# Performance work log

Measured on AMD Instinct MI355X. Metric: run time of the kernel, lower is better.

Reference implementation:

```python
import jax, jax.numpy as jnp
import numpy as np

D = 256       # d_model
NH = 8        # heads
K = 7         # neighborhood kernel size
DFF = 1024    # feedforward dim
EPS = 1e-5
B, H, W = 4, 56, 56


def layer_norm(x, g, b):
    m = jnp.mean(x, axis=-1, keepdims=True)
    v = jnp.mean((x - m) ** 2, axis=-1, keepdims=True)
    return (x - m) * jax.lax.rsqrt(v + EPS) * g + b


def neighborhood_attn(x, W_qkv, b_qkv, W_proj, b_proj):
    # NATTEN NeighborhoodAttention2D: each query attends to a KxK window
    # centered on it, clamped (shifted) at borders so every query sees K*K keys.
    Bx, Hx, Wx, C = x.shape
    hd = C // NH
    qkv = x @ W_qkv + b_qkv                      # [B,H,W,3C]
    q, k, v = jnp.split(qkv, 3, axis=-1)
    q = q.reshape(Bx, Hx, Wx, NH, hd)
    k = k.reshape(Bx, Hx, Wx, NH, hd)
    v = v.reshape(Bx, Hx, Wx, NH, hd)
    # neighbor index grids: start = clip(i - K//2, 0, H-K), window = start + [0..K)
    ih = jnp.clip(jnp.arange(Hx) - K // 2, 0, Hx - K)[:, None] + jnp.arange(K)  # [H,K]
    iw = jnp.clip(jnp.arange(Wx) - K // 2, 0, Wx - K)[:, None] + jnp.arange(K)  # [W,K]
    # gather K/V neighborhoods -> [B,H,W,K,K,NH,hd]
    k_nb = k[:, ih[:, None, :, None], iw[None, :, None, :]]
    v_nb = v[:, ih[:, None, :, None], iw[None, :, None, :]]
    attn = jnp.einsum('bhwnd,bhwijnd->bhwnij', q, k_nb) * (hd ** -0.5)
    attn = jax.nn.softmax(attn.reshape(Bx, Hx, Wx, NH, K * K), axis=-1)
    attn = attn.reshape(Bx, Hx, Wx, NH, K, K)
    out = jnp.einsum('bhwnij,bhwijnd->bhwnd', attn, v_nb).reshape(Bx, Hx, Wx, C)
    return out @ W_proj + b_proj


def setup_inputs() -> dict:
    key = jax.random.key(0)
    ks = jax.random.split(key, 8)
    s = 0.02
    return {
        'x': jax.random.normal(ks[0], (B, H, W, D), dtype=jnp.float32),
        'W_qkv': jax.random.normal(ks[1], (D, 3 * D), dtype=jnp.float32) * s,
        'b_qkv': jnp.zeros((3 * D,), dtype=jnp.float32),
        'W_proj': jax.random.normal(ks[2], (D, D), dtype=jnp.float32) * s,
        'b_proj': jnp.zeros((D,), dtype=jnp.float32),
        'W1': jax.random.normal(ks[3], (D, DFF), dtype=jnp.float32) * s,
        'b1': jnp.zeros((DFF,), dtype=jnp.float32),
        'W2': jax.random.normal(ks[4], (DFF, D), dtype=jnp.float32) * s,
        'b2': jnp.zeros((D,), dtype=jnp.float32),
        'g1': jnp.ones((D,), dtype=jnp.float32),
        'be1': jnp.zeros((D,), dtype=jnp.float32),
        'g2': jnp.ones((D,), dtype=jnp.float32),
        'be2': jnp.zeros((D,), dtype=jnp.float32),
    }


def reference(x, W_qkv, b_qkv, W_proj, b_proj, W1, b1, W2, b2, g1, be1, g2, be2):
    # norm_first=False (post-norm): x = norm1(x + mha(x)); x = norm2(x + ff(x))
    a = neighborhood_attn(x, W_qkv, b_qkv, W_proj, b_proj)
    x = layer_norm(x + a, g1, be1)
    f = jax.nn.relu(x @ W1 + b1) @ W2 + b2
    return layer_norm(x + f, g2, be2)
```

## Files before the change

### kernel.cpp

```cpp
#include <hip/hip_runtime.h>
#include <math.h>

#define BATCH 4
#define HH 56
#define WW 56
#define DMODEL 256
#define NHEADS 8
#define HD 32
#define NNB 49
#define NTOK (BATCH*HH*WW)

#define HALO 22
#define NHTOK (HALO*HALO)
#define KV_PAD 40

typedef __attribute__((ext_vector_type(8))) short s16x8;
typedef __attribute__((ext_vector_type(4))) float f32x4;
typedef __attribute__((ext_vector_type(2))) float f32x2;

__device__ inline unsigned short f2b(float f) {
    union { float f; unsigned int u; } v; v.f = f;
    unsigned int r = v.u + 0x7FFF + ((v.u >> 16) & 1);
    return (unsigned short)(r >> 16);
}
__device__ inline float b2f(unsigned short u) {
    union { float f; unsigned int u; } v; v.u = ((unsigned int)u) << 16;
    return v.f;
}

__device__ __forceinline__ f32x2 unpk(unsigned int u) {
    union { unsigned int u; float f; } lo, hi;
    lo.u = u << 16;
    hi.u = u & 0xffff0000u;
    return f32x2{lo.f, hi.f};
}

__device__ __forceinline__ f32x2 pk_fma(f32x2 a, f32x2 b, f32x2 c) {
#if __has_builtin(__builtin_elementwise_fma)
    return __builtin_elementwise_fma(a, b, c);
#else
    return f32x2{fmaf(a.x, b.x, c.x), fmaf(a.y, b.y, c.y)};
#endif
}

__device__ __forceinline__ void async16(const unsigned short* g, unsigned short* l) {
    __builtin_amdgcn_global_load_lds(
        (const __attribute__((address_space(1))) unsigned int*)g,
        (__attribute__((address_space(3))) unsigned int*)l, 16, 0, 0);
}

#define XCAST_BLOCKS 1568

__device__ __forceinline__ void transpose_tile(
    const float* __restrict__ src, unsigned short* __restrict__ dst,
    int K, int N, int kt, int nt, int tid, float* lds )
{
    const int k0 = kt * 64, n0 = nt * 64;
    #pragma unroll
    for (int p = 0; p < 4; ++p) {
        const int r  = p * 16 + (tid >> 4);
        const int c4 = (tid & 15) * 4;
        const float4 v = *(const float4*)(src + (size_t)(k0 + r) * N + n0 + c4);
        lds[r * 65 + c4 + 0] = v.x; lds[r * 65 + c4 + 1] = v.y;
        lds[r * 65 + c4 + 2] = v.z; lds[r * 65 + c4 + 3] = v.w;
    }
    __syncthreads();
    #pragma unroll
    for (int p = 0; p < 4; ++p) {
        const int c  = p * 16 + (tid >> 4);
        const int k4 = (tid & 15) * 4;
        ushort4 o;
        o.x = f2b(lds[(k4 + 0) * 65 + c]);
        o.y = f2b(lds[(k4 + 1) * 65 + c]);
        o.z = f2b(lds[(k4 + 2) * 65 + c]);
        o.w = f2b(lds[(k4 + 3) * 65 + c]);
        *(ushort4*)(dst + (size_t)(n0 + c) * K + k0 + k4) = o;
    }
}

__global__ __launch_bounds__(256)
void prep_kernel(const float* __restrict__ x,
                 const float* __restrict__ Wq, const float* __restrict__ Wp,
                 const float* __restrict__ W1, const float* __restrict__ W2,
                 unsigned short* __restrict__ xb,
                 unsigned short* __restrict__ Wqb, unsigned short* __restrict__ Wpb,
                 unsigned short* __restrict__ W1b, unsigned short* __restrict__ W2b)
{
    __shared__ float lds[64 * 65];
    const int tid = threadIdx.x;
    if (blockIdx.x < XCAST_BLOCKS) {
        const int i = blockIdx.x * 256 + tid;
        const float4* xp = (const float4*)x + (size_t)i * 2;
        const float4 a = xp[0], b = xp[1];
        s16x8 o;
        o[0] = (short)f2b(a.x); o[1] = (short)f2b(a.y);
        o[2] = (short)f2b(a.z); o[3] = (short)f2b(a.w);
        o[4] = (short)f2b(b.x); o[5] = (short)f2b(b.y);
        o[6] = (short)f2b(b.z); o[7] = (short)f2b(b.w);
        *((s16x8*)xb + i) = o;
        return;
    }
    int wb = blockIdx.x - XCAST_BLOCKS;
    if (wb < 48) {
        transpose_tile(Wq, Wqb, 256, 768, wb & 3, wb >> 2, tid, lds);
    } else if ((wb -= 48) < 16) {
        transpose_tile(Wp, Wpb, 256, 256, wb & 3, wb >> 2, tid, lds);
    } else if ((wb -= 16) < 64) {
        transpose_tile(W1, W1b, 256, 1024, wb & 3, wb >> 2, tid, lds);
    } else {
        wb -= 64;
        transpose_tile(W2, W2b, 1024, 256, wb & 15, wb >> 4, tid, lds);
    }
}

template<int BN>
__global__ __launch_bounds__(256)
void gemm_k(const unsigned short* __restrict__ Ab,
            const unsigned short* __restrict__ Bt, const float* __restrict__ bias,
            float* __restrict__ outf, unsigned short* __restrict__ outb,
            int M, int N, int K, int relu)
{
    constexpr int NB  = BN / 32;
    constexpr int BPW = BN / 32;
    __shared__ unsigned short As[2][128 * 64];
    __shared__ unsigned short Bs[2][BN * 64];

    const int tid = threadIdx.x;
    const int bm = blockIdx.y * 128, bn = blockIdx.x * BN;
    const int wid = tid >> 6, lane = tid & 63;
    const int wm = (wid >> 1) * 64, wn = (wid & 1) * (BN / 2);
    const int row16 = lane & 15, quad = lane >> 4;
    const int crow = lane >> 3, ck8 = (lane & 7) * 8;

    f32x4 acc[4][NB] = {};

    auto stage = [&](int buf, int k0) {
        #pragma unroll
        for (int c = 0; c < 4; ++c) {
            const int ch = wid * 4 + c;
            async16(Ab + (size_t)(bm + ch * 8 + crow) * K + k0 + ck8, As[buf] + ch * 512);
        }
        #pragma unroll
        for (int c = 0; c < BPW; ++c) {
            const int ch = wid * BPW + c;
            async16(Bt + (size_t)(bn + ch * 8 + crow) * K + k0 + ck8, Bs[buf] + ch * 512);
        }
    };
    auto compute = [&](int buf) {
        #pragma unroll
        for (int kc = 0; kc < 2; ++kc) {
            s16x8 af[4], bf[NB];
            #pragma unroll
            for (int i = 0; i < 4; ++i)
                af[i] = *(const s16x8*)(As[buf] + (wm + i * 16 + row16) * 64 + kc * 32 + quad * 8);
            #pragma unroll
            for (int j = 0; j < NB; ++j)
                bf[j] = *(const s16x8*)(Bs[buf] + (wn + j * 16 + row16) * 64 + kc * 32 + quad * 8);
            #pragma unroll
            for (int i = 0; i < 4; ++i)
                #pragma unroll
                for (int j = 0; j < NB; ++j)
                    acc[i][j] = __builtin_amdgcn_mfma_f32_16x16x32_bf16(af[i], bf[j], acc[i][j], 0, 0, 0);
        }
    };

    stage(0, 0);
    __syncthreads();
    for (int k0 = 0; k0 < K; k0 += 128) {
        stage(1, k0 + 64);
        compute(0);
        __syncthreads();
        if (k0 + 128 < K) stage(0, k0 + 128);
        compute(1);
        __syncthreads();
    }

    #pragma unroll
    for (int j = 0; j < NB; ++j) {
        const int col = bn + wn + j * 16 + row16;
        const float bb = bias[col];
        #pragma unroll
        for (int i = 0; i < 4; ++i) {
            const int r0 = bm + wm + i * 16 + quad * 4;
            #pragma unroll
            for (int reg = 0; reg < 4; ++reg) {
                float v = acc[i][j][reg] + bb;
                if (relu) v = fmaxf(v, 0.f);
                if (outf) outf[(size_t)(r0 + reg) * N + col] = v;
                if (outb) outb[(size_t)(r0 + reg) * N + col] = f2b(v);
            }
        }
    }
}

__global__ __launch_bounds__(512)
void gemm_ln(const unsigned short* __restrict__ Ab, const unsigned short* __restrict__ Bt,
             const float* __restrict__ bias, const float* __restrict__ resid,
             const float* __restrict__ g, const float* __restrict__ beta,
             float* __restrict__ outf, unsigned short* __restrict__ outb, int K)
{
    __shared__ unsigned short As[2][64 * 64];
    __shared__ unsigned short Bs[2][256 * 64];

    const int tid = threadIdx.x;
    const int bm = blockIdx.x * 64;
    const int wid = tid >> 6, lane = tid & 63;
    const int wm = (wid >> 2) * 32, wn = (wid & 3) * 64;
    const int wc = wid & 3;
    const int row16 = lane & 15, quad = lane >> 4;
    const int crow = lane >> 3, ck8 = (lane & 7) * 8;

    f32x4 acc[2][4] = {};

    auto stage = [&](int buf, int k0) {
        #pragma unroll
        for (int c = 0; c < 5; ++c) {
            const int ch = wid * 5 + c;
            if (ch < 8) {
                async16(Ab + (size_t)(bm + ch * 8 + crow) * K + k0 + ck8, As[buf] + ch * 512);
            } else {
                const int bc = ch - 8;
                async16(Bt + (size_t)(bc * 8 + crow) * K + k0 + ck8, Bs[buf] + bc * 512);
            }
        }
    };
    auto compute = [&](int buf) {
        #pragma unroll
        for (int kc = 0; kc < 2; ++kc) {
            s16x8 af[2], bf[4];
            #pragma unroll
            for (int i = 0; i < 2; ++i)
                af[i] = *(const s16x8*)(As[buf] + (wm + i * 16 + row16) * 64 + kc * 32 + quad * 8);
            #pragma unroll
            for (int j = 0; j < 4; ++j)
                bf[j] = *(const s16x8*)(Bs[buf] + (wn + j * 16 + row16) * 64 + kc * 32 + quad * 8);
            #pragma unroll
            for (int i = 0; i < 2; ++i)
                #pragma unroll
                for (int j = 0; j < 4; ++j)
                    acc[i][j] = __builtin_amdgcn_mfma_f32_16x16x32_bf16(af[i], bf[j], acc[i][j], 0, 0, 0);
        }
    };

    stage(0, 0);
    __syncthreads();
    for (int k0 = 0; k0 < K; k0 += 128) {
        stage(1, k0 + 64);
        compute(0);
        __syncthreads();
        if (k0 + 128 < K) stage(0, k0 + 128);
        compute(1);
        __syncthreads();
    }

    float bb[4], gv[4], bev[4];
    #pragma unroll
    for (int j = 0; j < 4; ++j) {
        const int col = wn + j * 16 + row16;
        bb[j] = bias[col]; gv[j] = g[col]; bev[j] = beta[col];
    }
    #pragma unroll
    for (int i = 0; i < 2; ++i) {
        #pragma unroll
        for (int reg = 0; reg < 4; ++reg) {
            const size_t rb = (size_t)(bm + wm + i * 16 + quad * 4 + reg) * 256;
            #pragma unroll
            for (int j = 0; j < 4; ++j)
                acc[i][j][reg] += bb[j] + resid[rb + wn + j * 16 + row16];
        }
    }

    float* red = (float*)As[0];
    #pragma unroll
    for (int i = 0; i < 2; ++i) {
        #pragma unroll
        for (int reg = 0; reg < 4; ++reg) {
            float s1 = 0.f, s2 = 0.f;
            #pragma unroll
            for (int j = 0; j < 4; ++j) {
                const float t = acc[i][j][reg];
                s1 += t; s2 += t * t;
            }
            #pragma unroll
            for (int o = 1; o < 16; o <<= 1) {
                s1 += __shfl_xor(s1, o, 64);
                s2 += __shfl_xor(s2, o, 64);
            }
            if (row16 == 0) {
                const int lrow = wm + i * 16 + quad * 4 + reg;
                red[lrow * 8 + wc * 2]     = s1;
                red[lrow * 8 + wc * 2 + 1] = s2;
            }
        }
    }
    __syncthreads();
    float* stats = red + 512;
    if (tid < 64) {
        const float S1 = red[tid*8] + red[tid*8+2] + red[tid*8+4] + red[tid*8+6];
        const float S2 = red[tid*8+1] + red[tid*8+3] + red[tid*8+5] + red[tid*8+7];
        const float m = S1 * (1.0f / 256.0f);
        const float var = S2 * (1.0f / 256.0f) - m * m;
        stats[tid * 2]     = m;
        stats[tid * 2 + 1] = rsqrtf(var + 1e-5f);
    }
    __syncthreads();

    #pragma unroll
    for (int i = 0; i < 2; ++i) {
        #pragma unroll
        for (int reg = 0; reg < 4; ++reg) {
            const int lrow = wm + i * 16 + quad * 4 + reg;
            const float m = stats[lrow * 2], r = stats[lrow * 2 + 1];
            const size_t rb = (size_t)(bm + lrow) * 256;
            #pragma unroll
            for (int j = 0; j < 4; ++j) {
                const int col = wn + j * 16 + row16;
                const float o = (acc[i][j][reg] - m) * r * gv[j] + bev[j];
                outf[rb + col] = o;
                if (outb) outb[rb + col] = f2b(o);
            }
        }
    }
}

__global__ __launch_bounds__(256, 2)
void natt_kernel(const unsigned short* __restrict__ qkvb, unsigned short* __restrict__ att)
{
    const int blk  = blockIdx.x;
    const int head = blk & 7;
    const int t2   = blk >> 3;
    const int tile = t2 & 15;
    const int b    = t2 >> 4;
    const int r0 = (tile >> 2) * 16, c0 = (tile & 3) * 16;
    const int hs = min(max(r0 - 3, 0), 34);
    const int ws = min(max(c0 - 3, 0), 34);

    __shared__ unsigned short Ks[NHTOK * KV_PAD];
    __shared__ unsigned short Vs[NHTOK * KV_PAD];

    const int tid = threadIdx.x;

    #pragma unroll
    for (int it = 0; it < 8; ++it) {
        const int t = it * 64 + (tid >> 2);
        if (t < NHTOK) {
            const int hr = t / HALO, hc = t - hr * HALO;
            const size_t rb = ((size_t)((b * 56 + hs + hr) * 56 + (ws + hc))) * 768;
            const int d8 = (tid & 3) * 8;
            *(s16x8*)(Ks + t * KV_PAD + d8) = *(const s16x8*)(qkvb + rb + 256 + head * 32 + d8);
            *(s16x8*)(Vs + t * KV_PAD + d8) = *(const s16x8*)(qkvb + rb + 512 + head * 32 + d8);
        }
    }

    const int qh = min(r0 + (tid >> 4), 55);
    const int qw = min(c0 + (tid & 15), 55);
    const int tok = (b * 56 + qh) * 56 + qw;
    const int ro = min(max(qh - 3, 0), 49) - hs;
    const int co = min(max(qw - 3, 0), 49) - ws;

    f32x2 qf[16];
    {
        const unsigned int* qp = (const unsigned int*)(qkvb + (size_t)tok * 768 + head * 32);
        #pragma unroll
        for (int p = 0; p < 16; ++p)
            qf[p] = unpk(qp[p]) * 0.17677669529663687f;
    }
    __syncthreads();

    f32x2 acc[16] = {};
    float sum = 0.f;
    for (int i = 0; i < 7; ++i) {
        const int trow = (ro + i) * HALO + co;
        #pragma unroll
        for (int j = 0; j < 7; ++j) {
            const unsigned int* kp = (const unsigned int*)(Ks + (trow + j) * KV_PAD);
            const unsigned int* vp = (const unsigned int*)(Vs + (trow + j) * KV_PAD);
            const uint4 ka = *(const uint4*)(kp);
            const uint4 kb = *(const uint4*)(kp + 4);
            const uint4 kc = *(const uint4*)(kp + 8);
            const uint4 kd = *(const uint4*)(kp + 12);
            const uint4 va = *(const uint4*)(vp);
            const uint4 vb = *(const uint4*)(vp + 4);
            const uint4 vc = *(const uint4*)(vp + 8);
            const uint4 vd = *(const uint4*)(vp + 12);
            f32x2 sa = {0.f, 0.f}, sb = {0.f, 0.f};
            sa = pk_fma(qf[0],  unpk(ka.x), sa);  sb = pk_fma(qf[1],  unpk(ka.y), sb);
            sa = pk_fma(qf[2],  unpk(ka.z), sa);  sb = pk_fma(qf[3],  unpk(ka.w), sb);
            sa = pk_fma(qf[4],  unpk(kb.x), sa);  sb = pk_fma(qf[5],  unpk(kb.y), sb);
            sa = pk_fma(qf[6],  unpk(kb.z), sa);  sb = pk_fma(qf[7],  unpk(kb.w), sb);
            sa = pk_fma(qf[8],  unpk(kc.x), sa);  sb = pk_fma(qf[9],  unpk(kc.y), sb);
            sa = pk_fma(qf[10], unpk(kc.z), sa);  sb = pk_fma(qf[11], unpk(kc.w), sb);
            sa = pk_fma(qf[12], unpk(kd.x), sa);  sb = pk_fma(qf[13], unpk(kd.y), sb);
            sa = pk_fma(qf[14], unpk(kd.z), sa);  sb = pk_fma(qf[15], unpk(kd.w), sb);
            const float p = __expf(sa.x + sa.y + sb.x + sb.y);
            sum += p;
            const f32x2 pv = {p, p};
            acc[0]  = pk_fma(pv, unpk(va.x), acc[0]);
            acc[1]  = pk_fma(pv, unpk(va.y), acc[1]);
            acc[2]  = pk_fma(pv, unpk(va.z), acc[2]);
            acc[3]  = pk_fma(pv, unpk(va.w), acc[3]);
            acc[4]  = pk_fma(pv, unpk(vb.x), acc[4]);
            acc[5]  = pk_fma(pv, unpk(vb.y), acc[5]);
            acc[6]  = pk_fma(pv, unpk(vb.z), acc[6]);
            acc[7]  = pk_fma(pv, unpk(vb.w), acc[7]);
            acc[8]  = pk_fma(pv, unpk(vc.x), acc[8]);
            acc[9]  = pk_fma(pv, unpk(vc.y), acc[9]);
            acc[10] = pk_fma(pv, unpk(vc.z), acc[10]);
            acc[11] = pk_fma(pv, unpk(vc.w), acc[11]);
            acc[12] = pk_fma(pv, unpk(vd.x), acc[12]);
            acc[13] = pk_fma(pv, unpk(vd.y), acc[13]);
            acc[14] = pk_fma(pv, unpk(vd.z), acc[14]);
            acc[15] = pk_fma(pv, unpk(vd.w), acc[15]);
        }
    }
    const float inv = 1.0f / sum;

    unsigned short* op = att + (size_t)tok * DMODEL + head * 32;
    #pragma unroll
    for (int d4 = 0; d4 < 8; ++d4) {
        ushort4 o;
        o.x = f2b(acc[d4 * 2].x     * inv);
        o.y = f2b(acc[d4 * 2].y     * inv);
        o.z = f2b(acc[d4 * 2 + 1].x * inv);
        o.w = f2b(acc[d4 * 2 + 1].y * inv);
        *(ushort4*)(op + d4 * 4) = o;
    }
}

extern "C" void kernel_launch(void* const* d_in, const int* in_sizes, int n_in,
                              void* d_out, int out_size, void* d_ws, size_t ws_size,
                              hipStream_t stream)
{
    const float* x      = (const float*)d_in[0];
    const float* W_qkv  = (const float*)d_in[1];
    const float* b_qkv  = (const float*)d_in[2];
    const float* W_proj = (const float*)d_in[3];
    const float* b_proj = (const float*)d_in[4];
    const float* W1     = (const float*)d_in[5];
    const float* b1     = (const float*)d_in[6];
    const float* W2     = (const float*)d_in[7];
    const float* b2     = (const float*)d_in[8];
    const float* g1     = (const float*)d_in[9];
    const float* be1    = (const float*)d_in[10];
    const float* g2     = (const float*)d_in[11];
    const float* be2    = (const float*)d_in[12];
    float* out = (float*)d_out;

    char* ws = (char*)d_ws;
    const int M = NTOK;

    unsigned short* qkvb = (unsigned short*)ws;
    unsigned short* h    = (unsigned short*)ws;
    unsigned short* attb = (unsigned short*)(ws + 38535168);
    float*          xn   = (float*)(ws + 57802752);
    unsigned short* xnb  = (unsigned short*)(ws + 70647808);
    unsigned short* Wqb  = (unsigned short*)(ws + 77070336);
    unsigned short* Wpb  = Wqb + 196608;
    unsigned short* W1b  = Wpb + 65536;
    unsigned short* W2b  = W1b + 262144;
    unsigned short* xb   = (unsigned short*)(ws + 78643200);

    dim3 blk(256);

    prep_kernel<<<dim3(XCAST_BLOCKS + 48 + 16 + 64 + 64), blk, 0, stream>>>(
        x, W_qkv, W_proj, W1, W2, xb, Wqb, Wpb, W1b, W2b);

    gemm_k<128><<<dim3(6, 98), blk, 0, stream>>>(xb, Wqb, b_qkv, nullptr, qkvb, M, 768, 256, 0);

    natt_kernel<<<dim3(512), blk, 0, stream>>>(qkvb, attb);

    gemm_ln<<<dim3(M / 64), dim3(512), 0, stream>>>(attb, Wpb, b_proj, x, g1, be1, xn, xnb, 256);

    gemm_k<128><<<dim3(8, 98), blk, 0, stream>>>(xnb, W1b, b1, nullptr, h, M, 1024, 256, 1);

    gemm_ln<<<dim3(M / 64), dim3(512), 0, stream>>>(h, W2b, b2, xn, g2, be2, out, nullptr, 1024);
}
```

Measured before the change: 194.8 us.

## Swizzle GEMM LDS tiles, remap blocks per XCD, stage epilogue through LDS

XOR-swizzles the 16-byte chunks of the LDS A/B tiles in both GEMM kernels so the fragment reads avoid bank conflicts. Remaps the 1D grid so consecutive tiles land on the same XCD, aiming for better L2 reuse of shared A/B rows. The bf16 epilogue of gemm_k now writes to LDS first, then stores coalesced 16-byte vectors to global memory, replacing scattered 2-byte stores. This costs an extra barrier and LDS pass, and the template parameter and fp32 output path are dropped.

```diff
diff --git a/kernel.cpp b/kernel.cpp
--- a/kernel.cpp
+++ b/kernel.cpp
@@ -113,53 +113,60 @@
     }
 }
 
-template<int BN>
 __global__ __launch_bounds__(256)
 void gemm_k(const unsigned short* __restrict__ Ab,
             const unsigned short* __restrict__ Bt, const float* __restrict__ bias,
-            float* __restrict__ outf, unsigned short* __restrict__ outb,
-            int M, int N, int K, int relu)
-{
-    constexpr int NB  = BN / 32;
-    constexpr int BPW = BN / 32;
+            unsigned short* __restrict__ outb,
+            int N, int K, int relu)
+{
     __shared__ unsigned short As[2][128 * 64];
-    __shared__ unsigned short Bs[2][BN * 64];
+    __shared__ unsigned short Bs[2][128 * 64];
 
     const int tid = threadIdx.x;
-    const int bm = blockIdx.y * 128, bn = blockIdx.x * BN;
+
+    const int nwg = gridDim.x;
+    const int q8 = nwg >> 3, r8 = nwg & 7;
+    const int xcd = blockIdx.x & 7, pos = blockIdx.x >> 3;
+    const int d = (xcd < r8 ? xcd * (q8 + 1) : r8 * (q8 + 1) + (xcd - r8) * q8) + pos;
+    const int nbx = N >> 7;
+    const int bm = (d / nbx) * 128, bn = (d % nbx) * 128;
+
     const int wid = tid >> 6, lane = tid & 63;
-    const int wm = (wid >> 1) * 64, wn = (wid & 1) * (BN / 2);
+    const int wm = (wid >> 1) * 64, wn = (wid & 1) * 64;
     const int row16 = lane & 15, quad = lane >> 4;
-    const int crow = lane >> 3, ck8 = (lane & 7) * 8;
-
-    f32x4 acc[4][NB] = {};
+    const int crow = lane >> 3;
+    const int ckS = ((lane & 7) ^ crow) * 8;
+
+    f32x4 acc[4][4] = {};
 
     auto stage = [&](int buf, int k0) {
         #pragma unroll
         for (int c = 0; c < 4; ++c) {
             const int ch = wid * 4 + c;
-            async16(Ab + (size_t)(bm + ch * 8 + crow) * K + k0 + ck8, As[buf] + ch * 512);
-        }
-        #pragma unroll
-        for (int c = 0; c < BPW; ++c) {
-            const int ch = wid * BPW + c;
-            async16(Bt + (size_t)(bn + ch * 8 + crow) * K + k0 + ck8, Bs[buf] + ch * 512);
+            async16(Ab + (size_t)(bm + ch * 8 + crow) * K + k0 + ckS, As[buf] + ch * 512);
+        }
+        #pragma unroll
+        for (int c = 0; c < 4; ++c) {
+            const int ch = wid * 4 + c;
+            async16(Bt + (size_t)(bn + ch * 8 + crow) * K + k0 + ckS, Bs[buf] + ch * 512);
         }
     };
     auto compute = [&](int buf) {
         #pragma unroll
         for (int kc = 0; kc < 2; ++kc) {
-            s16x8 af[4], bf[NB];
+            s16x8 af[4], bf[4];
             #pragma unroll
             for (int i = 0; i < 4; ++i)
-                af[i] = *(const s16x8*)(As[buf] + (wm + i * 16 + row16) * 64 + kc * 32 + quad * 8);
-            #pragma unroll
-            for (int j = 0; j < NB; ++j)
-                bf[j] = *(const s16x8*)(Bs[buf] + (wn + j * 16 + row16) * 64 + kc * 32 + quad * 8);
+                af[i] = *(const s16x8*)(As[buf] + (wm + i * 16 + row16) * 64
+                                        + (((kc * 4 + quad) ^ (row16 & 7)) * 8));
+            #pragma unroll
+            for (int j = 0; j < 4; ++j)
+                bf[j] = *(const s16x8*)(Bs[buf] + (wn + j * 16 + row16) * 64
+                                        + (((kc * 4 + quad) ^ (row16 & 7)) * 8));
             #pragma unroll
             for (int i = 0; i < 4; ++i)
                 #pragma unroll
-                for (int j = 0; j < NB; ++j)
+                for (int j = 0; j < 4; ++j)
                     acc[i][j] = __builtin_amdgcn_mfma_f32_16x16x32_bf16(af[i], bf[j], acc[i][j], 0, 0, 0);
         }
     };
@@ -175,21 +182,28 @@
         __syncthreads();
     }
 
-    #pragma unroll
-    for (int j = 0; j < NB; ++j) {
-        const int col = bn + wn + j * 16 + row16;
-        const float bb = bias[col];
+    unsigned short* Cs = (unsigned short*)As;
+    #pragma unroll
+    for (int j = 0; j < 4; ++j) {
+        const int col = wn + j * 16 + row16;
+        const float bb = bias[bn + col];
         #pragma unroll
         for (int i = 0; i < 4; ++i) {
-            const int r0 = bm + wm + i * 16 + quad * 4;
+            const int rr = wm + i * 16 + quad * 4;
             #pragma unroll
             for (int reg = 0; reg < 4; ++reg) {
                 float v = acc[i][j][reg] + bb;
                 if (relu) v = fmaxf(v, 0.f);
-                if (outf) outf[(size_t)(r0 + reg) * N + col] = v;
-                if (outb) outb[(size_t)(r0 + reg) * N + col] = f2b(v);
-            }
-        }
+                Cs[(rr + reg) * 128 + col] = f2b(v);
+            }
+        }
+    }
+    __syncthreads();
+    #pragma unroll
+    for (int p = 0; p < 8; ++p) {
+        const int s = p * 256 + tid;
+        const int rr = s >> 4, cb = (s & 15) * 8;
+        *(s16x8*)(outb + (size_t)(bm + rr) * N + bn + cb) = *(const s16x8*)(Cs + rr * 128 + cb);
     }
 }
 
@@ -208,7 +222,8 @@
     const int wm = (wid >> 2) * 32, wn = (wid & 3) * 64;
     const int wc = wid & 3;
     const int row16 = lane & 15, quad = lane >> 4;
-    const int crow = lane >> 3, ck8 = (lane & 7) * 8;
+    const int crow = lane >> 3;
+    const int ckS = ((lane & 7) ^ crow) * 8;
 
     f32x4 acc[2][4] = {};
 
@@ -217,10 +232,10 @@
         for (int c = 0; c < 5; ++c) {
             const int ch = wid * 5 + c;
             if (ch < 8) {
-                async16(Ab + (size_t)(bm + ch * 8 + crow) * K + k0 + ck8, As[buf] + ch * 512);
+                async16(Ab + (size_t)(bm + ch * 8 + crow) * K + k0 + ckS, As[buf] + ch * 512);
             } else {
                 const int bc = ch - 8;
-                async16(Bt + (size_t)(bc * 8 + crow) * K + k0 + ck8, Bs[buf] + bc * 512);
+                async16(Bt + (size_t)(bc * 8 + crow) * K + k0 + ckS, Bs[buf] + bc * 512);
             }
         }
     };
@@ -230,10 +245,12 @@
             s16x8 af[2], bf[4];
             #pragma unroll
             for (int i = 0; i < 2; ++i)
-                af[i] = *(const s16x8*)(As[buf] + (wm + i * 16 + row16) * 64 + kc * 32 + quad * 8);
+                af[i] = *(const s16x8*)(As[buf] + (wm + i * 16 + row16) * 64
+                                        + (((kc * 4 + quad) ^ (row16 & 7)) * 8));
             #pragma unroll
             for (int j = 0; j < 4; ++j)
-                bf[j] = *(const s16x8*)(Bs[buf] + (wn + j * 16 + row16) * 64 + kc * 32 + quad * 8);
+                bf[j] = *(const s16x8*)(Bs[buf] + (wn + j * 16 + row16) * 64
+                                        + (((kc * 4 + quad) ^ (row16 & 7)) * 8));
             #pragma unroll
             for (int i = 0; i < 2; ++i)
                 #pragma unroll
@@ -465,13 +482,13 @@
     prep_kernel<<<dim3(XCAST_BLOCKS + 48 + 16 + 64 + 64), blk, 0, stream>>>(
         x, W_qkv, W_proj, W1, W2, xb, Wqb, Wpb, W1b, W2b);
 
-    gemm_k<128><<<dim3(6, 98), blk, 0, stream>>>(xb, Wqb, b_qkv, nullptr, qkvb, M, 768, 256, 0);
+    gemm_k<<<dim3(6 * 98), blk, 0, stream>>>(xb, Wqb, b_qkv, qkvb, 768, 256, 0);
 
     natt_kernel<<<dim3(512), blk, 0, stream>>>(qkvb, attb);
 
     gemm_ln<<<dim3(M / 64), dim3(512), 0, stream>>>(attb, Wpb, b_proj, x, g1, be1, xn, xnb, 256);
 
-    gemm_k<128><<<dim3(8, 98), blk, 0, stream>>>(xnb, W1b, b1, nullptr, h, M, 1024, 256, 1);
+    gemm_k<<<dim3(8 * 98), blk, 0, stream>>>(xnb, W1b, b1, h, 1024, 256, 1);
 
     gemm_ln<<<dim3(M / 64), dim3(512), 0, stream>>>(h, W2b, b2, xn, g2, be2, out, nullptr, 1024);
 }
```

After: 178.3 us. 1.09x faster.
